# Optimization experiments

Measured on AMD Instinct MI355X. Metric: run time of the kernel, lower is better.

The kernel has to match this reference:

```python
import jax, jax.numpy as jnp
import numpy as np
from jax import lax

D_MODEL = 1024
D_STATE = 16
D_CONV = 4
D_INNER = 2 * D_MODEL
BATCH = 2
SEQ = 1024


def setup_inputs() -> dict:
    key = jax.random.key(0)
    ks = jax.random.split(key, 8)
    std = 0.02
    return {
        "x": jax.random.normal(ks[0], (BATCH, SEQ, D_MODEL), jnp.float32),
        "in_proj_w": jax.random.normal(ks[1], (2 * D_INNER, D_MODEL), jnp.float32) * std,
        "conv_w": jax.random.normal(ks[2], (D_INNER, 1, D_CONV), jnp.float32) * 0.1,
        "x_proj_w": jax.random.normal(ks[3], (D_STATE + 1, D_INNER), jnp.float32) * std,
        "dt_w": jax.random.normal(ks[4], (D_INNER, 1), jnp.float32) * std,
        "dt_b": jnp.zeros((D_INNER,), jnp.float32),
        "A_param": jax.random.normal(ks[5], (D_INNER, D_STATE), jnp.float32) * std,
        "D_param": jnp.ones((D_INNER,), jnp.float32),
        "out_w": jax.random.normal(ks[6], (D_MODEL, D_INNER), jnp.float32) * std,
        "out_b": jnp.zeros((D_MODEL,), jnp.float32),
    }


def _silu(v):
    return v * jax.nn.sigmoid(v)


def _mamba_forward(x, in_proj_w, conv_w, x_proj_w, dt_w, dt_b, A_param, D_param, out_w, out_b):
    B, L, _ = x.shape
    # in_proj: [B,L,2*d_inner]
    xz = jnp.einsum('bld,ed->ble', x, in_proj_w)
    u, z = jnp.split(xz, 2, axis=-1)  # each [B,L,d_inner]
    # depthwise causal conv1d along time
    uc = u.transpose(0, 2, 1)  # [B,d_inner,L]
    uc = lax.conv_general_dilated(
        uc, conv_w, window_strides=(1,), padding=[(D_CONV - 1, D_CONV - 1)],
        dimension_numbers=('NCH', 'OIH', 'NCH'), feature_group_count=D_INNER,
    )[:, :, :L]
    u = _silu(uc.transpose(0, 2, 1))  # [B,L,d_inner]
    # x_proj -> (dt scalar, B coeffs)
    x_dbl = jnp.einsum('bld,ed->ble', u, x_proj_w)  # [B,L,d_state+1]
    dt_in = x_dbl[..., :1]                          # [B,L,1]
    Bmat = x_dbl[..., 1:]                           # [B,L,d_state]
    delta = jax.nn.softplus(dt_in * dt_w[:, 0] + dt_b)  # [B,L,d_inner]
    A = -jnp.exp(A_param)                            # [d_inner,d_state]

    # selective scan (time-major lax.scan)
    def step(h, inp):
        d_t, b_t = inp  # [B,d_inner], [B,d_state]
        h = jnp.exp(A * d_t[..., None]) * h + d_t[..., None] * b_t[:, None, :]
        y = jnp.einsum('bdn,bn->bd', h, b_t)
        return h, y

    h0 = jnp.zeros((B, D_INNER, D_STATE), x.dtype)
    _, ys = lax.scan(step, h0, (delta.transpose(1, 0, 2), Bmat.transpose(1, 0, 2)))
    y = ys.transpose(1, 0, 2) + u * D_param  # [B,L,d_inner]
    y = y * _silu(z)
    return jnp.einsum('bld,ed->ble', y, out_w) + out_b


def reference(x, in_proj_w, conv_w, x_proj_w, dt_w, dt_b, A_param, D_param, out_w, out_b):
    return _mamba_forward(x, in_proj_w, conv_w, x_proj_w, dt_w, dt_b, A_param, D_param, out_w, out_b)
```

## Files before the change

kernel.cpp:

```cpp
#include <hip/hip_runtime.h>
#include <stdint.h>
#include <stddef.h>

#define D_MODEL 1024
#define D_STATE 16
#define D_INNER 2048
#define BATCH   2
#define SEQ     1024
#define MROWS   (BATCH*SEQ)

#define NCH 64
#define TCH (SEQ/NCH)
#define NREC (BATCH*D_INNER*D_STATE)

#define XKS 8
#define XKC (D_INNER/XKS)

typedef __bf16 bf16x8 __attribute__((ext_vector_type(8)));
typedef float  f32x4  __attribute__((ext_vector_type(4)));
typedef unsigned short u16x8 __attribute__((ext_vector_type(8)));

__device__ __forceinline__ unsigned short f2bf(float f) {
    unsigned int u = __float_as_uint(f);
    u += 0x7fffu + ((u >> 16) & 1u);
    return (unsigned short)(u >> 16);
}
__device__ __forceinline__ float bf2f(unsigned short v) {
    return __uint_as_float((unsigned int)v << 16);
}

__device__ __forceinline__ void gl_lds16(const unsigned short* g, unsigned short* l) {
    __builtin_amdgcn_global_load_lds(
        (const __attribute__((address_space(1))) unsigned int*)g,
        (__attribute__((address_space(3))) unsigned int*)l, 16, 0, 0);
}

__global__ void cvt_all_kernel(const float* __restrict__ x,
                               const float* __restrict__ w1,
                               const float* __restrict__ w2,
                               const float* __restrict__ xw,
                               unsigned short* __restrict__ xb,
                               unsigned short* __restrict__ wbi,
                               unsigned short* __restrict__ wbo,
                               unsigned short* __restrict__ wbp) {
    int blk = blockIdx.x, tid = threadIdx.x;
    if (blk < 8192) {
        const float* src; unsigned short* dst; int i;
        if (blk < 2048)      { src = x;  dst = xb;  i = blk * 1024 + tid * 4; }
        else if (blk < 6144) { src = w1; dst = wbi; i = (blk - 2048) * 1024 + tid * 4; }
        else                 { src = w2; dst = wbo; i = (blk - 6144) * 1024 + tid * 4; }
        float4 v = *(const float4*)(src + i);
        ushort4 o;
        o.x = f2bf(v.x); o.y = f2bf(v.y); o.z = f2bf(v.z); o.w = f2bf(v.w);
        *(ushort4*)(dst + i) = o;
    } else {
        int id = (blk - 8192) * 256 + tid;
        wbp[id] = (id < 17 * D_INNER) ? f2bf(xw[id]) : (unsigned short)0;
    }
}

template<int NT, bool SPLITK2, bool OUT_BF16>
__global__ void gemm_bf16_kernel(const unsigned short* __restrict__ A,
                                 const unsigned short* __restrict__ Bw,
                                 void* __restrict__ Cv,
                                 int M, int N, int K) {
    constexpr int NTW = NT / 32;
    constexpr int BCH = NT / 8;
    constexpr int LPW = 4 + BCH / 4;
    __shared__ __align__(16) unsigned short Al[2][2 * 128 * 32];
    __shared__ __align__(16) unsigned short Bl[2][2 * NT * 32];

    const int tid  = threadIdx.x;
    const int lane = tid & 63;
    const int wid  = tid >> 6;
    const int wm   = wid >> 1;
    const int wn   = wid & 1;
    const int ln   = lane & 15;
    const int q    = lane >> 4;
    const int mblk = blockIdx.y * 128;
    const int nblk = blockIdx.x * NT;
    const int srow = lane >> 2;
    const int spart = lane & 3;

    const int kbeg = SPLITK2 ? blockIdx.z * (K / 2) : 0;
    const int kend = SPLITK2 ? kbeg + K / 2 : K;

    f32x4 acc[4][NTW] = {};

    auto stage = [&](int buf, int k0) {
        #pragma unroll
        for (int h = 0; h < 4; ++h) {
            int j = wid * 4 + h;
            int kh = j & 1, rb = j >> 1;
            int row = rb * 16 + srow;
            gl_lds16(A + (size_t)(mblk + row) * K + k0 + kh * 32 + spart * 8,
                     Al[buf] + kh * 4096 + rb * 512);
        }
        #pragma unroll
        for (int h = 0; h < BCH / 4; ++h) {
            int j = wid * (BCH / 4) + h;
            int kh = j & 1, rb = j >> 1;
            int row = rb * 16 + srow;
            gl_lds16(Bw + (size_t)(nblk + row) * K + k0 + kh * 32 + spart * 8,
                     Bl[buf] + kh * (NT * 32) + rb * 512);
        }
    };

    const int niter = (kend - kbeg) >> 6;
    stage(0, kbeg);
    int cur = 0;

    for (int it = 0; it < niter; ++it) {
        int k0 = kbeg + (it << 6);
        if (it + 1 < niter) {
            stage(cur ^ 1, k0 + 64);
            if constexpr (LPW == 8) asm volatile("s_waitcnt vmcnt(8)" ::: "memory");
            else                    asm volatile("s_waitcnt vmcnt(6)" ::: "memory");
        } else {
            asm volatile("s_waitcnt vmcnt(0)" ::: "memory");
        }
        __builtin_amdgcn_sched_barrier(0);
        __builtin_amdgcn_s_barrier();
        __builtin_amdgcn_sched_barrier(0);

        #pragma unroll
        for (int kh = 0; kh < 2; ++kh) {
            bf16x8 af[4], bfr[NTW];
            #pragma unroll
            for (int mt = 0; mt < 4; ++mt)
                af[mt] = *(const bf16x8*)(Al[cur] + kh * 4096 + (wm * 64 + mt * 16 + ln) * 32 + q * 8);
            #pragma unroll
            for (int nt = 0; nt < NTW; ++nt)
                bfr[nt] = *(const bf16x8*)(Bl[cur] + kh * (NT * 32) + (wn * (NT/2) + nt * 16 + ln) * 32 + q * 8);
            #pragma unroll
            for (int mt = 0; mt < 4; ++mt)
                #pragma unroll
                for (int nt = 0; nt < NTW; ++nt)
                    acc[mt][nt] = __builtin_amdgcn_mfma_f32_16x16x32_bf16(
                        af[mt], bfr[nt], acc[mt][nt], 0, 0, 0);
        }

        __builtin_amdgcn_sched_barrier(0);
        __builtin_amdgcn_s_barrier();
        cur ^= 1;
    }

    size_t cofs = SPLITK2 ? (size_t)blockIdx.z * M * N : 0;
    #pragma unroll
    for (int mt = 0; mt < 4; ++mt) {
        #pragma unroll
        for (int nt = 0; nt < NTW; ++nt) {
            int col = nblk + wn * (NT/2) + nt * 16 + ln;
            #pragma unroll
            for (int r = 0; r < 4; ++r) {
                int row = mblk + wm * 64 + mt * 16 + q * 4 + r;
                if (OUT_BF16)
                    ((unsigned short*)Cv)[cofs + (size_t)row * N + col] = f2bf(acc[mt][nt][r]);
                else
                    ((float*)Cv)[cofs + (size_t)row * N + col] = acc[mt][nt][r];
            }
        }
    }
}

__global__ void splitk_reduce_kernel(const float* __restrict__ part,
                                     const float* __restrict__ bias,
                                     float* __restrict__ out) {
    int i = (blockIdx.x * 256 + threadIdx.x) * 4;
    int n = i & (D_MODEL - 1);
    float4 a = *(const float4*)(part + i);
    float4 b = *(const float4*)(part + (size_t)MROWS * D_MODEL + i);
    float4 bv = *(const float4*)(bias + n);
    float4 o;
    o.x = a.x + b.x + bv.x; o.y = a.y + b.y + bv.y;
    o.z = a.z + b.z + bv.z; o.w = a.w + b.w + bv.w;
    *(float4*)(out + i) = o;
}

__global__ void conv_silu_kernel(const unsigned short* __restrict__ xzb,
                                 const float* __restrict__ conv_w,
                                 unsigned short* __restrict__ ub) {
    int idx = blockIdx.x * 256 + threadIdx.x;
    int d8 = idx & 255;
    int m = idx >> 8;
    int l = m & (SEQ - 1);
    int d = d8 * 8;
    const float4* wv = (const float4*)(conv_w + (size_t)d * 4);
    float4 w[8];
    #pragma unroll
    for (int e = 0; e < 8; ++e) w[e] = wv[e];
    float s[8] = {0.f, 0.f, 0.f, 0.f, 0.f, 0.f, 0.f, 0.f};
    #pragma unroll
    for (int j = 0; j < 4; ++j) {
        if (l - j >= 0) {
            u16x8 r = *(const u16x8*)(xzb + (size_t)(m - j) * 4096 + d);
            #pragma unroll
            for (int e = 0; e < 8; ++e) {
                float wt = (j == 0) ? w[e].w : (j == 1) ? w[e].z
                         : (j == 2) ? w[e].y : w[e].x;
                s[e] += wt * bf2f(r[e]);
            }
        }
    }
    u16x8 o;
    #pragma unroll
    for (int e = 0; e < 8; ++e) {
        float sig = 1.f / (1.f + __expf(-s[e]));
        o[e] = f2bf(s[e] * sig);
    }
    *(u16x8*)(ub + (size_t)m * D_INNER + d) = o;
}

__global__ void xproj_mfma_kernel(const unsigned short* __restrict__ ub,
                                  const unsigned short* __restrict__ wbp,
                                  float* __restrict__ part) {
    __shared__ __align__(16) unsigned short Al[2][64 * 64];
    __shared__ __align__(16) unsigned short Bl[2][32 * 64];

    const int tid  = threadIdx.x;
    const int lane = tid & 63;
    const int wid  = tid >> 6;
    const int ln   = lane & 15;
    const int q    = lane >> 4;
    const int m0   = blockIdx.y * 64;
    const int ks   = blockIdx.x;
    const int srow = lane >> 3;
    const int spart = lane & 7;

    f32x4 acc[2] = {};

    auto stage = [&](int buf, int it) {
        int k0 = ks * XKC + it * 64;
        #pragma unroll
        for (int h = 0; h < 2; ++h) {
            int j = wid * 2 + h;
            int row = j * 8 + srow;
            gl_lds16(ub + (size_t)(m0 + row) * D_INNER + k0 + spart * 8, Al[buf] + j * 512);
        }
        {
            int row = wid * 8 + srow;
            gl_lds16(wbp + (size_t)row * D_INNER + k0 + spart * 8, Bl[buf] + wid * 512);
        }
    };

    stage(0, 0);
    __syncthreads();
    int cur = 0;

    for (int it = 0; it < 4; ++it) {
        if (it < 3) stage(cur ^ 1, it + 1);

        bf16x8 af[2], bfr[2][2];
        #pragma unroll
        for (int kh = 0; kh < 2; ++kh) {
            af[kh] = *(const bf16x8*)(Al[cur] + (wid * 16 + ln) * 64 + kh * 32 + q * 8);
            bfr[0][kh] = *(const bf16x8*)(Bl[cur] + (0 * 16 + ln) * 64 + kh * 32 + q * 8);
            bfr[1][kh] = *(const bf16x8*)(Bl[cur] + (1 * 16 + ln) * 64 + kh * 32 + q * 8);
        }
        #pragma unroll
        for (int kh = 0; kh < 2; ++kh) {
            acc[0] = __builtin_amdgcn_mfma_f32_16x16x32_bf16(af[kh], bfr[0][kh], acc[0], 0, 0, 0);
            acc[1] = __builtin_amdgcn_mfma_f32_16x16x32_bf16(af[kh], bfr[1][kh], acc[1], 0, 0, 0);
        }
        __syncthreads();
        cur ^= 1;
    }

    #pragma unroll
    for (int nf = 0; nf < 2; ++nf) {
        #pragma unroll
        for (int r = 0; r < 4; ++r) {
            int m = m0 + wid * 16 + q * 4 + r;
            part[((size_t)ks * MROWS + m) * 32 + nf * 16 + ln] = acc[nf][r];
        }
    }
}

__global__ void xproj_reduce_kernel(const float* __restrict__ part,
                                    float* __restrict__ dti,
                                    float* __restrict__ Bm) {
    int id = blockIdx.x * 256 + threadIdx.x;
    int m = id >> 5, n = id & 31;
    float s = 0.f;
    #pragma unroll
    for (int ks = 0; ks < XKS; ++ks) s += part[(size_t)ks * MROWS * 32 + id];
    if (n == 0) dti[m] = s;
    else if (n < 17) Bm[(size_t)m * D_STATE + (n - 1)] = s;
}

__device__ __forceinline__ float softplus_f(float xv) {
    return fmaxf(xv, 0.f) + __logf(1.f + __expf(-fabsf(xv)));
}

__global__ void scanA_kernel(const float* __restrict__ dt_in,
                             const float* __restrict__ Bm,
                             const float* __restrict__ dt_w,
                             const float* __restrict__ dt_b,
                             const float* __restrict__ A_param,
                             float* __restrict__ Pg,
                             float* __restrict__ Sg) {
    __shared__ float sdt[TCH];
    __shared__ float sB[TCH * D_STATE];
    const int tid = threadIdx.x;
    const int b = blockIdx.z, c = blockIdx.y;
    const int d = blockIdx.x * 256 + tid;

    if (tid < TCH) sdt[tid] = dt_in[b * SEQ + c * TCH + tid];
    if (tid < TCH * D_STATE / 4)
        ((float4*)sB)[tid] = ((const float4*)(Bm + ((size_t)(b * SEQ + c * TCH)) * D_STATE))[tid];
    __syncthreads();

    const float dtw = dt_w[d], dtb = dt_b[d];
    float aA[D_STATE], h[D_STATE];
    #pragma unroll
    for (int n4 = 0; n4 < 4; ++n4) {
        float4 ap = ((const float4*)(A_param + (size_t)d * D_STATE))[n4];
        aA[n4*4+0] = -__expf(ap.x); aA[n4*4+1] = -__expf(ap.y);
        aA[n4*4+2] = -__expf(ap.z); aA[n4*4+3] = -__expf(ap.w);
    }
    #pragma unroll
    for (int n = 0; n < D_STATE; ++n) h[n] = 0.f;
    float tsum = 0.f;

    for (int t = 0; t < TCH; ++t) {
        float sp = softplus_f(sdt[t] * dtw + dtb);
        tsum += sp;
        #pragma unroll
        for (int n = 0; n < D_STATE; ++n) {
            float a = __expf(aA[n] * sp);
            h[n] = a * h[n] + sp * sB[t * D_STATE + n];
        }
    }

    size_t base = (size_t)c * NREC + ((size_t)(b * D_INNER + d)) * D_STATE;
    #pragma unroll
    for (int n4 = 0; n4 < 4; ++n4) {
        float4 pv, sv;
        pv.x = __expf(aA[n4*4+0] * tsum); pv.y = __expf(aA[n4*4+1] * tsum);
        pv.z = __expf(aA[n4*4+2] * tsum); pv.w = __expf(aA[n4*4+3] * tsum);
        sv.x = h[n4*4+0]; sv.y = h[n4*4+1]; sv.z = h[n4*4+2]; sv.w = h[n4*4+3];
        *(float4*)(Pg + base + n4 * 4) = pv;
        *(float4*)(Sg + base + n4 * 4) = sv;
    }
}

__global__ void scanB_kernel(const float* __restrict__ Pg,
                             const float* __restrict__ Sg,
                             float* __restrict__ Hin) {
    int idx = blockIdx.x * 256 + threadIdx.x;
    float h = 0.f;
    #pragma unroll
    for (int c = 0; c < NCH; ++c) {
        size_t o = (size_t)c * NREC + idx;
        Hin[o] = h;
        h = Pg[o] * h + Sg[o];
    }
}

__global__ void scanC_kernel(const float* __restrict__ dt_in,
                             const float* __restrict__ Bm,
                             const float* __restrict__ dt_w,
                             const float* __restrict__ dt_b,
                             const float* __restrict__ A_param,
                             const float* __restrict__ Hin,
                             const unsigned short* __restrict__ ub,
                             const unsigned short* __restrict__ xzb,
                             const float* __restrict__ Dp,
                             unsigned short* __restrict__ ypb) {
    __shared__ float sdt[TCH];
    __shared__ float sB[TCH * D_STATE];
    const int tid = threadIdx.x;
    const int b = blockIdx.z, c = blockIdx.y;
    const int d = blockIdx.x * 256 + tid;

    if (tid < TCH) sdt[tid] = dt_in[b * SEQ + c * TCH + tid];
    if (tid < TCH * D_STATE / 4)
        ((float4*)sB)[tid] = ((const float4*)(Bm + ((size_t)(b * SEQ + c * TCH)) * D_STATE))[tid];
    __syncthreads();

    const float dtw = dt_w[d], dtb = dt_b[d];
    const float Dv = Dp[d];
    float aA[D_STATE], h[D_STATE];
    #pragma unroll
    for (int n4 = 0; n4 < 4; ++n4) {
        float4 ap = ((const float4*)(A_param + (size_t)d * D_STATE))[n4];
        aA[n4*4+0] = -__expf(ap.x); aA[n4*4+1] = -__expf(ap.y);
        aA[n4*4+2] = -__expf(ap.z); aA[n4*4+3] = -__expf(ap.w);
    }
    size_t hbase = (size_t)c * NREC + ((size_t)(b * D_INNER + d)) * D_STATE;
    #pragma unroll
    for (int n4 = 0; n4 < 4; ++n4) {
        float4 hv = *(const float4*)(Hin + hbase + n4 * 4);
        h[n4*4+0] = hv.x; h[n4*4+1] = hv.y; h[n4*4+2] = hv.z; h[n4*4+3] = hv.w;
    }

    const size_t mrow0 = (size_t)b * SEQ + c * TCH;
    for (int t = 0; t < TCH; ++t) {
        float sp = softplus_f(sdt[t] * dtw + dtb);
        float y0 = 0.f, y1 = 0.f, y2 = 0.f, y3 = 0.f;
        #pragma unroll
        for (int n4 = 0; n4 < 4; ++n4) {
            #pragma unroll
            for (int j = 0; j < 4; ++j) {
                int n = n4 * 4 + j;
                float Bv = sB[t * D_STATE + n];
                float a = __expf(aA[n] * sp);
                h[n] = a * h[n] + sp * Bv;
                float p = h[n] * Bv;
                if (n4 == 0) y0 += p; else if (n4 == 1) y1 += p;
                else if (n4 == 2) y2 += p; else y3 += p;
            }
        }
        float y = (y0 + y1) + (y2 + y3);
        size_t m = mrow0 + t;
        float z  = bf2f(xzb[m * 4096 + D_INNER + d]);
        float sz = z / (1.f + __expf(-z));
        float uv = bf2f(ub[m * D_INNER + d]);
        ypb[m * D_INNER + d] = f2bf((y + uv * Dv) * sz);
    }
}

extern "C" void kernel_launch(void* const* d_in, const int* in_sizes, int n_in,
                              void* d_out, int out_size, void* d_ws, size_t ws_size,
                              hipStream_t stream) {
    const float* x         = (const float*)d_in[0];
    const float* in_proj_w = (const float*)d_in[1];
    const float* conv_w    = (const float*)d_in[2];
    const float* x_proj_w  = (const float*)d_in[3];
    const float* dt_w      = (const float*)d_in[4];
    const float* dt_b      = (const float*)d_in[5];
    const float* A_param   = (const float*)d_in[6];
    const float* D_param   = (const float*)d_in[7];
    const float* out_w     = (const float*)d_in[8];
    const float* out_b     = (const float*)d_in[9];
    float* out = (float*)d_out;

    char* ws = (char*)d_ws;
    unsigned short* xb  = (unsigned short*)(ws);
    unsigned short* wbi = (unsigned short*)(ws + (4u  << 20));
    unsigned short* wbo = (unsigned short*)(ws + (12u << 20));
    unsigned short* xzb = (unsigned short*)(ws + (16u << 20));
    unsigned short* ub  = (unsigned short*)(ws + (32u << 20));
    float*          dti = (float*)(ws + (40u << 20));
    float*          Bm  = (float*)(ws + (40u << 20) + (64u  << 10));
    unsigned short* wbp = (unsigned short*)(ws + (40u << 20) + (192u << 10));
    float*          xpt = (float*)(ws + (40u << 20) + (512u << 10));
    float*          Pg  = (float*)(ws + (44u  << 20));
    float*          Sg  = (float*)(ws + (60u  << 20));
    float*          Hin = (float*)(ws + (76u  << 20));
    unsigned short* ypb = (unsigned short*)(ws + (92u  << 20));
    float*          g2p = (float*)(ws + (100u << 20));

    cvt_all_kernel<<<dim3(8448), 256, 0, stream>>>(
        x, in_proj_w, out_w, x_proj_w, xb, wbi, wbo, wbp);

    gemm_bf16_kernel<128, false, true><<<dim3(4096 / 128, MROWS / 128), 256, 0, stream>>>(
        xb, wbi, xzb, MROWS, 2 * D_INNER, D_MODEL);

    conv_silu_kernel<<<dim3(MROWS), 256, 0, stream>>>(xzb, conv_w, ub);

    xproj_mfma_kernel<<<dim3(XKS, MROWS / 64), 256, 0, stream>>>(ub, wbp, xpt);
    xproj_reduce_kernel<<<dim3(MROWS * 32 / 256), 256, 0, stream>>>(xpt, dti, Bm);

    scanA_kernel<<<dim3(D_INNER / 256, NCH, BATCH), 256, 0, stream>>>(
        dti, Bm, dt_w, dt_b, A_param, Pg, Sg);
    scanB_kernel<<<dim3(NREC / 256), 256, 0, stream>>>(Pg, Sg, Hin);
    scanC_kernel<<<dim3(D_INNER / 256, NCH, BATCH), 256, 0, stream>>>(
        dti, Bm, dt_w, dt_b, A_param, Hin, ub, xzb, D_param, ypb);

    gemm_bf16_kernel<64, true, false><<<dim3(1024 / 64, MROWS / 128, 2), 256, 0, stream>>>(
        ypb, wbo, g2p, MROWS, D_MODEL, D_INNER);

    splitk_reduce_kernel<<<dim3(MROWS * D_MODEL / 1024), 256, 0, stream>>>(g2p, out_b, out);
}
```

Baseline: 225.0 us.

## Replace split-K reduce kernels with atomics, precompute -exp(A), halve scan chunks

Removes the split-K reduction kernels for the output GEMM and the x_proj GEMM. Partial sums are now accumulated with atomicAdd into the output, which is pre-initialised with the bias, and into zeroed dt/B buffers, all set up in the conversion kernel. -exp(A) is computed once in the conversion kernel instead of in every scan block, and the scan chunk count drops from 64 to 32, which shrinks the chunk-state buffers. This saves launches and partial-buffer traffic, at the cost of atomic contention, non-deterministic summation order, and longer serial chunks in the scan.

```diff
diff --git a/kernel.cpp b/kernel.cpp
--- a/kernel.cpp
+++ b/kernel.cpp
@@ -9,7 +9,7 @@
 #define SEQ     1024
 #define MROWS   (BATCH*SEQ)
 
-#define NCH 64
+#define NCH 32
 #define TCH (SEQ/NCH)
 #define NREC (BATCH*D_INNER*D_STATE)
 
@@ -39,10 +39,16 @@
                                const float* __restrict__ w1,
                                const float* __restrict__ w2,
                                const float* __restrict__ xw,
+                               const float* __restrict__ ob,
+                               const float* __restrict__ Ap,
                                unsigned short* __restrict__ xb,
                                unsigned short* __restrict__ wbi,
                                unsigned short* __restrict__ wbo,
-                               unsigned short* __restrict__ wbp) {
+                               unsigned short* __restrict__ wbp,
+                               float* __restrict__ outp,
+                               float* __restrict__ aAg,
+                               float* __restrict__ dti,
+                               float* __restrict__ Bm) {
     int blk = blockIdx.x, tid = threadIdx.x;
     if (blk < 8192) {
         const float* src; unsigned short* dst; int i;
@@ -53,9 +59,26 @@
         ushort4 o;
         o.x = f2bf(v.x); o.y = f2bf(v.y); o.z = f2bf(v.z); o.w = f2bf(v.w);
         *(ushort4*)(dst + i) = o;
-    } else {
+    } else if (blk < 8448) {
         int id = (blk - 8192) * 256 + tid;
         wbp[id] = (id < 17 * D_INNER) ? f2bf(xw[id]) : (unsigned short)0;
+    } else if (blk < 10496) {
+        int i = (blk - 8448) * 1024 + tid * 4;
+        int n = i & (D_MODEL - 1);
+        *(float4*)(outp + i) = *(const float4*)(ob + n);
+    } else if (blk < 10528) {
+        int i = (blk - 10496) * 1024 + tid * 4;
+        float4 a = *(const float4*)(Ap + i);
+        float4 r;
+        r.x = -__expf(a.x); r.y = -__expf(a.y);
+        r.z = -__expf(a.z); r.w = -__expf(a.w);
+        *(float4*)(aAg + i) = r;
+    } else if (blk < 10530) {
+        int i = (blk - 10528) * 1024 + tid * 4;
+        *(float4*)(dti + i) = float4{0.f, 0.f, 0.f, 0.f};
+    } else {
+        int i = (blk - 10530) * 1024 + tid * 4;
+        *(float4*)(Bm + i) = float4{0.f, 0.f, 0.f, 0.f};
     }
 }
 
@@ -145,7 +168,6 @@
         cur ^= 1;
     }
 
-    size_t cofs = SPLITK2 ? (size_t)blockIdx.z * M * N : 0;
     #pragma unroll
     for (int mt = 0; mt < 4; ++mt) {
         #pragma unroll
@@ -154,27 +176,16 @@
             #pragma unroll
             for (int r = 0; r < 4; ++r) {
                 int row = mblk + wm * 64 + mt * 16 + q * 4 + r;
-                if (OUT_BF16)
-                    ((unsigned short*)Cv)[cofs + (size_t)row * N + col] = f2bf(acc[mt][nt][r]);
-                else
-                    ((float*)Cv)[cofs + (size_t)row * N + col] = acc[mt][nt][r];
+                if (SPLITK2) {
+                    atomicAdd((float*)Cv + (size_t)row * N + col, acc[mt][nt][r]);
+                } else if (OUT_BF16) {
+                    ((unsigned short*)Cv)[(size_t)row * N + col] = f2bf(acc[mt][nt][r]);
+                } else {
+                    ((float*)Cv)[(size_t)row * N + col] = acc[mt][nt][r];
+                }
             }
         }
     }
-}
-
-__global__ void splitk_reduce_kernel(const float* __restrict__ part,
-                                     const float* __restrict__ bias,
-                                     float* __restrict__ out) {
-    int i = (blockIdx.x * 256 + threadIdx.x) * 4;
-    int n = i & (D_MODEL - 1);
-    float4 a = *(const float4*)(part + i);
-    float4 b = *(const float4*)(part + (size_t)MROWS * D_MODEL + i);
-    float4 bv = *(const float4*)(bias + n);
-    float4 o;
-    o.x = a.x + b.x + bv.x; o.y = a.y + b.y + bv.y;
-    o.z = a.z + b.z + bv.z; o.w = a.w + b.w + bv.w;
-    *(float4*)(out + i) = o;
 }
 
 __global__ void conv_silu_kernel(const unsigned short* __restrict__ xzb,
@@ -213,7 +224,8 @@
 
 __global__ void xproj_mfma_kernel(const unsigned short* __restrict__ ub,
                                   const unsigned short* __restrict__ wbp,
-                                  float* __restrict__ part) {
+                                  float* __restrict__ dti,
+                                  float* __restrict__ Bm) {
     __shared__ __align__(16) unsigned short Al[2][64 * 64];
     __shared__ __align__(16) unsigned short Bl[2][32 * 64];
 
@@ -268,24 +280,14 @@
 
     #pragma unroll
     for (int nf = 0; nf < 2; ++nf) {
+        int col = nf * 16 + ln;
         #pragma unroll
         for (int r = 0; r < 4; ++r) {
             int m = m0 + wid * 16 + q * 4 + r;
-            part[((size_t)ks * MROWS + m) * 32 + nf * 16 + ln] = acc[nf][r];
-        }
-    }
-}
-
-__global__ void xproj_reduce_kernel(const float* __restrict__ part,
-                                    float* __restrict__ dti,
-                                    float* __restrict__ Bm) {
-    int id = blockIdx.x * 256 + threadIdx.x;
-    int m = id >> 5, n = id & 31;
-    float s = 0.f;
-    #pragma unroll
-    for (int ks = 0; ks < XKS; ++ks) s += part[(size_t)ks * MROWS * 32 + id];
-    if (n == 0) dti[m] = s;
-    else if (n < 17) Bm[(size_t)m * D_STATE + (n - 1)] = s;
+            if (col == 0)       atomicAdd(dti + m, acc[nf][r]);
+            else if (col < 17)  atomicAdd(Bm + (size_t)m * D_STATE + (col - 1), acc[nf][r]);
+        }
+    }
 }
 
 __device__ __forceinline__ float softplus_f(float xv) {
@@ -296,7 +298,7 @@
                              const float* __restrict__ Bm,
                              const float* __restrict__ dt_w,
                              const float* __restrict__ dt_b,
-                             const float* __restrict__ A_param,
+                             const float* __restrict__ aAg,
                              float* __restrict__ Pg,
                              float* __restrict__ Sg) {
     __shared__ float sdt[TCH];
@@ -314,9 +316,9 @@
     float aA[D_STATE], h[D_STATE];
     #pragma unroll
     for (int n4 = 0; n4 < 4; ++n4) {
-        float4 ap = ((const float4*)(A_param + (size_t)d * D_STATE))[n4];
-        aA[n4*4+0] = -__expf(ap.x); aA[n4*4+1] = -__expf(ap.y);
-        aA[n4*4+2] = -__expf(ap.z); aA[n4*4+3] = -__expf(ap.w);
+        float4 av = ((const float4*)(aAg + (size_t)d * D_STATE))[n4];
+        aA[n4*4+0] = av.x; aA[n4*4+1] = av.y;
+        aA[n4*4+2] = av.z; aA[n4*4+3] = av.w;
     }
     #pragma unroll
     for (int n = 0; n < D_STATE; ++n) h[n] = 0.f;
@@ -361,7 +363,7 @@
                              const float* __restrict__ Bm,
                              const float* __restrict__ dt_w,
                              const float* __restrict__ dt_b,
-                             const float* __restrict__ A_param,
+                             const float* __restrict__ aAg,
                              const float* __restrict__ Hin,
                              const unsigned short* __restrict__ ub,
                              const unsigned short* __restrict__ xzb,
@@ -383,9 +385,9 @@
     float aA[D_STATE], h[D_STATE];
     #pragma unroll
     for (int n4 = 0; n4 < 4; ++n4) {
-        float4 ap = ((const float4*)(A_param + (size_t)d * D_STATE))[n4];
-        aA[n4*4+0] = -__expf(ap.x); aA[n4*4+1] = -__expf(ap.y);
-        aA[n4*4+2] = -__expf(ap.z); aA[n4*4+3] = -__expf(ap.w);
+        float4 av = ((const float4*)(aAg + (size_t)d * D_STATE))[n4];
+        aA[n4*4+0] = av.x; aA[n4*4+1] = av.y;
+        aA[n4*4+2] = av.z; aA[n4*4+3] = av.w;
     }
     size_t hbase = (size_t)c * NREC + ((size_t)(b * D_INNER + d)) * D_STATE;
     #pragma unroll
@@ -444,32 +446,29 @@
     float*          dti = (float*)(ws + (40u << 20));
     float*          Bm  = (float*)(ws + (40u << 20) + (64u  << 10));
     unsigned short* wbp = (unsigned short*)(ws + (40u << 20) + (192u << 10));
-    float*          xpt = (float*)(ws + (40u << 20) + (512u << 10));
-    float*          Pg  = (float*)(ws + (44u  << 20));
-    float*          Sg  = (float*)(ws + (60u  << 20));
-    float*          Hin = (float*)(ws + (76u  << 20));
-    unsigned short* ypb = (unsigned short*)(ws + (92u  << 20));
-    float*          g2p = (float*)(ws + (100u << 20));
-
-    cvt_all_kernel<<<dim3(8448), 256, 0, stream>>>(
-        x, in_proj_w, out_w, x_proj_w, xb, wbi, wbo, wbp);
+    float*          aAg = (float*)(ws + (40u << 20) + (320u << 10));
+    float*          Pg  = (float*)(ws + (44u << 20));
+    float*          Sg  = (float*)(ws + (52u << 20));
+    float*          Hin = (float*)(ws + (60u << 20));
+    unsigned short* ypb = (unsigned short*)(ws + (68u << 20));
+
+    cvt_all_kernel<<<dim3(10562), 256, 0, stream>>>(
+        x, in_proj_w, out_w, x_proj_w, out_b, A_param,
+        xb, wbi, wbo, wbp, out, aAg, dti, Bm);
 
     gemm_bf16_kernel<128, false, true><<<dim3(4096 / 128, MROWS / 128), 256, 0, stream>>>(
         xb, wbi, xzb, MROWS, 2 * D_INNER, D_MODEL);
 
     conv_silu_kernel<<<dim3(MROWS), 256, 0, stream>>>(xzb, conv_w, ub);
 
-    xproj_mfma_kernel<<<dim3(XKS, MROWS / 64), 256, 0, stream>>>(ub, wbp, xpt);
-    xproj_reduce_kernel<<<dim3(MROWS * 32 / 256), 256, 0, stream>>>(xpt, dti, Bm);
+    xproj_mfma_kernel<<<dim3(XKS, MROWS / 64), 256, 0, stream>>>(ub, wbp, dti, Bm);
 
     scanA_kernel<<<dim3(D_INNER / 256, NCH, BATCH), 256, 0, stream>>>(
-        dti, Bm, dt_w, dt_b, A_param, Pg, Sg);
+        dti, Bm, dt_w, dt_b, aAg, Pg, Sg);
     scanB_kernel<<<dim3(NREC / 256), 256, 0, stream>>>(Pg, Sg, Hin);
     scanC_kernel<<<dim3(D_INNER / 256, NCH, BATCH), 256, 0, stream>>>(
-        dti, Bm, dt_w, dt_b, A_param, Hin, ub, xzb, D_param, ypb);
+        dti, Bm, dt_w, dt_b, aAg, Hin, ub, xzb, D_param, ypb);
 
     gemm_bf16_kernel<64, true, false><<<dim3(1024 / 64, MROWS / 128, 2), 256, 0, stream>>>(
-        ypb, wbo, g2p, MROWS, D_MODEL, D_INNER);
-
-    splitk_reduce_kernel<<<dim3(MROWS * D_MODEL / 1024), 256, 0, stream>>>(g2p, out_b, out);
-}
+        ypb, wbo, out, MROWS, D_MODEL, D_INNER);
+}
```

Result: no change. 226.1 us (+0.5%).
